# Optimization experiments

Hardware: AMD Instinct MI355X
Metric: run time of the kernel (lower is better)

The kernel has to match this reference:

```python
import jax, jax.numpy as jnp
import numpy as np

N_PE = 100000   # num 'pe' nodes
N_R = 100000    # num 'router' nodes
E = 600000      # edges per relation
D_IN = 64       # input feature dim per node type
H = 128         # hidden_channels
G = 64          # graphs in batch


def setup_inputs() -> dict:
    key = jax.random.key(0)
    ks = jax.random.split(key, 20)
    inp = {}
    inp["x_pe"] = jax.random.normal(ks[0], (N_PE, D_IN), jnp.float32)
    inp["x_r"] = jax.random.normal(ks[1], (N_R, D_IN), jnp.float32)
    # edge_index per relation: row0 = src node ids, row1 = dst node ids
    inp["ei_per"] = jax.random.randint(ks[2], (2, E), 0, N_PE, jnp.int32)   # pe -> router
    inp["ei_rpe"] = jax.random.randint(ks[3], (2, E), 0, N_R, jnp.int32)    # router -> pe
    inp["ei_rr"] = jax.random.randint(ks[4], (2, E), 0, N_R, jnp.int32)     # router -> router
    inp["batch_pe"] = jnp.sort(jax.random.randint(ks[5], (N_PE,), 0, G, jnp.int32))
    inp["batch_r"] = jnp.sort(jax.random.randint(ks[6], (N_R,), 0, G, jnp.int32))
    # GraphConv params, relation axis ordered [pe->router, router->pe, router->router]
    s1 = 1.0 / np.sqrt(D_IN)
    s2 = 1.0 / np.sqrt(H)
    inp["Wrel1"] = jax.random.normal(ks[7], (3, D_IN, H), jnp.float32) * s1
    inp["brel1"] = jnp.zeros((3, H), jnp.float32)
    inp["Wroot1"] = jax.random.normal(ks[8], (3, D_IN, H), jnp.float32) * s1
    inp["Wrel23"] = jax.random.normal(ks[9], (2, 3, H, H), jnp.float32) * s2
    inp["brel23"] = jnp.zeros((2, 3, H), jnp.float32)
    inp["Wroot23"] = jax.random.normal(ks[10], (2, 3, H, H), jnp.float32) * s2
    # per-node-type MLP heads, type axis ordered [pe, router]
    inp["mlp_W1"] = jax.random.normal(ks[11], (2, H, 5), jnp.float32) * s2
    inp["mlp_b1"] = jnp.zeros((2, 5), jnp.float32)
    inp["mlp_W2"] = jax.random.normal(ks[12], (2, 5, 1), jnp.float32) * (1.0 / np.sqrt(5.0))
    inp["mlp_b2"] = jnp.zeros((2, 1), jnp.float32)
    inp["out_W"] = jax.random.normal(ks[13], (2, 1), jnp.float32) * (1.0 / np.sqrt(2.0))
    inp["out_b"] = jnp.zeros((1,), jnp.float32)
    return inp


def _hetero_graphconv(x_pe, x_r, ei_per, ei_rpe, ei_rr, Wrel, brel, Wroot):
    # GraphConv: lin_rel(scatter_add(x_src)) + lin_root(x_dst); to_hetero sums per dst type.
    agg_r_from_pe = jax.ops.segment_sum(x_pe[ei_per[0]], ei_per[1], num_segments=N_R)
    agg_pe_from_r = jax.ops.segment_sum(x_r[ei_rpe[0]], ei_rpe[1], num_segments=N_PE)
    agg_r_from_r = jax.ops.segment_sum(x_r[ei_rr[0]], ei_rr[1], num_segments=N_R)
    o_pe = agg_pe_from_r @ Wrel[1] + brel[1] + x_pe @ Wroot[1]
    o_r = (agg_r_from_pe @ Wrel[0] + brel[0] + x_r @ Wroot[0]) \
        + (agg_r_from_r @ Wrel[2] + brel[2] + x_r @ Wroot[2])
    return o_pe, o_r


def reference(x_pe, x_r, ei_per, ei_rpe, ei_rr, batch_pe, batch_r,
              Wrel1, brel1, Wroot1, Wrel23, brel23, Wroot23,
              mlp_W1, mlp_b1, mlp_W2, mlp_b2, out_W, out_b):
    h_pe, h_r = _hetero_graphconv(x_pe, x_r, ei_per, ei_rpe, ei_rr, Wrel1, brel1, Wroot1)
    h_pe, h_r = jax.nn.relu(h_pe), jax.nn.relu(h_r)
    h_pe, h_r = _hetero_graphconv(h_pe, h_r, ei_per, ei_rpe, ei_rr, Wrel23[0], brel23[0], Wroot23[0])
    h_pe, h_r = jax.nn.relu(h_pe), jax.nn.relu(h_r)
    h_pe, h_r = _hetero_graphconv(h_pe, h_r, ei_per, ei_rpe, ei_rr, Wrel23[1], brel23[1], Wroot23[1])
    gm_pe = jax.ops.segment_max(h_pe, batch_pe, num_segments=G)  # [G, H]
    gm_r = jax.ops.segment_max(h_r, batch_r, num_segments=G)
    def mlp(x, W1, b1, W2, b2):
        return jax.nn.relu(x @ W1 + b1) @ W2 + b2
    o_pe = mlp(gm_pe, mlp_W1[0], mlp_b1[0], mlp_W2[0], mlp_b2[0])  # [G, 1]
    o_r = mlp(gm_r, mlp_W1[1], mlp_b1[1], mlp_W2[1], mlp_b2[1])
    cat = jnp.concatenate([o_pe, o_r], axis=1)  # [G, 2]
    return cat @ out_W + out_b  # [G, 1]
```

## Files before the change

### kernel.cpp

```cpp
#include <hip/hip_runtime.h>
#include <cstddef>
#include <cstdint>

#define DIN 64
#define HID 128
#define NBKMAX 256
#define EPB 8192

typedef _Float16 half4v __attribute__((ext_vector_type(4)));
typedef _Float16 half8v __attribute__((ext_vector_type(8)));
typedef float f32x16 __attribute__((ext_vector_type(16)));

__device__ __forceinline__ unsigned encf(float f) {
    unsigned b = __float_as_uint(f);
    return (b & 0x80000000u) ? ~b : (b | 0x80000000u);
}
__device__ __forceinline__ float decf(unsigned u) {
    unsigned b = (u & 0x80000000u) ? (u & 0x7FFFFFFFu) : ~u;
    return __uint_as_float(b);
}

__global__ void matadd3_k(const float* a0, const float* b0f, float* o0, int n0,
                          const float* a1, const float* b1f, float* o1, int n1,
                          const float* a2, const float* b2f, float* o2, int n2) {
    int r = blockIdx.y;
    const float* a = r == 0 ? a0 : (r == 1 ? a1 : a2);
    const float* b = r == 0 ? b0f : (r == 1 ? b1f : b2f);
    float* o = r == 0 ? o0 : (r == 1 ? o1 : o2);
    int n = r == 0 ? n0 : (r == 1 ? n1 : n2);
    int i = blockIdx.x * 256 + threadIdx.x;
    if (i < n) o[i] = a[i] + b[i];
}

__global__ void conv_x2_k(const float* s0, _Float16* d0, int n40,
                          const float* s1, _Float16* d1, int n41) {
    int r = blockIdx.y;
    const float* s = r == 0 ? s0 : s1;
    _Float16* d = r == 0 ? d0 : d1;
    int n4 = r == 0 ? n40 : n41;
    int i = blockIdx.x * 256 + threadIdx.x;
    if (i >= n4) return;
    float4 v = *reinterpret_cast<const float4*>(&s[i * 4]);
    half4v h;
    h.x = (_Float16)v.x; h.y = (_Float16)v.y; h.z = (_Float16)v.z; h.w = (_Float16)v.w;
    *reinterpret_cast<half4v*>(&d[i * 4]) = h;
}

struct CW { const float* src; _Float16* dst; int K; int total; };
__global__ void conv_w7_k(CW c0, CW c1, CW c2, CW c3, CW c4, CW c5, CW c6) {
    CW J;
    switch (blockIdx.y) {
        case 0: J = c0; break; case 1: J = c1; break; case 2: J = c2; break;
        case 3: J = c3; break; case 4: J = c4; break; case 5: J = c5; break;
        default: J = c6; break;
    }
    int i = blockIdx.x * 256 + threadIdx.x;
    if (i >= J.total) return;
    int m = i / (J.K * HID);
    int rem = i % (J.K * HID);
    int k = rem / HID;
    int col = rem % HID;
    J.dst[(size_t)m * HID * J.K + (size_t)col * J.K + k] = (_Float16)J.src[i];
}

__global__ __launch_bounds__(256) void bhist_k(const int* e0, const int* e1, const int* e2, int E,
                                               int* c0, int* c1, int* c2) {
    int r = blockIdx.y;
    const int* ei = r == 0 ? e0 : (r == 1 ? e1 : e2);
    int* cnt = r == 0 ? c0 : (r == 1 ? c1 : c2);
    __shared__ int sc[NBKMAX];
    int t = threadIdx.x;
    sc[t] = 0;
    __syncthreads();
    int base = blockIdx.x * EPB;
    int n = min(EPB, E - base);
    for (int i = t; i < n; i += 256)
        atomicAdd(&sc[(unsigned)ei[E + base + i] >> 9], 1);
    __syncthreads();
    if (sc[t]) atomicAdd(&cnt[t], sc[t]);
}

__global__ __launch_bounds__(256) void bscan_k(int* c0, int* bb0, int* cu0, int* rp0, int n0,
                                               int* c1, int* bb1, int* cu1, int* rp1, int n1,
                                               int* c2, int* bb2, int* cu2, int* rp2, int n2,
                                               int E) {
    __shared__ int sh[256];
    int t = threadIdx.x;
    for (int r = 0; r < 3; ++r) {
        int* cnt = r == 0 ? c0 : (r == 1 ? c1 : c2);
        int* bb  = r == 0 ? bb0 : (r == 1 ? bb1 : bb2);
        int* cu  = r == 0 ? cu0 : (r == 1 ? cu1 : cu2);
        int* rp  = r == 0 ? rp0 : (r == 1 ? rp1 : rp2);
        int N    = r == 0 ? n0 : (r == 1 ? n1 : n2);
        int v = cnt[t];
        sh[t] = v;
        __syncthreads();
        for (int off = 1; off < 256; off <<= 1) {
            int val = (t >= off) ? sh[t - off] : 0;
            __syncthreads();
            sh[t] += val;
            __syncthreads();
        }
        int ex = sh[t] - v;
        bb[t] = ex;
        cu[t] = ex;
        if (t == 255) bb[256] = sh[255];
        if (t == 0) rp[N] = E;
        __syncthreads();
    }
}

__global__ __launch_bounds__(256) void bin_k(const int* e0, const int* e1, const int* e2, int E,
                                             int* cu0, int* cu1, int* cu2,
                                             unsigned* t0, unsigned* t1, unsigned* t2) {
    int r = blockIdx.y;
    const int* ei = r == 0 ? e0 : (r == 1 ? e1 : e2);
    int* gcur = r == 0 ? cu0 : (r == 1 ? cu1 : cu2);
    unsigned* temp = r == 0 ? t0 : (r == 1 ? t1 : t2);
    __shared__ unsigned pk[EPB];
    __shared__ unsigned short bkb[EPB];
    __shared__ int cnt[NBKMAX];
    __shared__ int scn[NBKMAX];
    __shared__ int rb[NBKMAX];
    int t = threadIdx.x;
    int base = blockIdx.x * EPB;
    int n = min(EPB, E - base);
    cnt[t] = 0;
    __syncthreads();
    for (int i = t; i < n; i += 256)
        atomicAdd(&cnt[(unsigned)ei[E + base + i] >> 9], 1);
    __syncthreads();
    {
        int v = cnt[t];
        scn[t] = v;
        __syncthreads();
        for (int off = 1; off < 256; off <<= 1) {
            int val = (t >= off) ? scn[t - off] : 0;
            __syncthreads();
            scn[t] += val;
            __syncthreads();
        }
        int ex = scn[t] - v;
        __syncthreads();
        scn[t] = ex;
    }
    {
        int c = cnt[t];
        rb[t] = c ? atomicAdd(&gcur[t], c) : 0;
        cnt[t] = 0;
    }
    __syncthreads();
    for (int i = t; i < n; i += 256) {
        int s = ei[base + i];
        int d = ei[E + base + i];
        int b = (unsigned)d >> 9;
        int slot = scn[b] + atomicAdd(&cnt[b], 1);
        pk[slot] = ((unsigned)s << 9) | (unsigned)(d & 511);
        bkb[slot] = (unsigned short)b;
    }
    __syncthreads();
    for (int i = t; i < n; i += 256) {
        int b = bkb[i];
        temp[rb[b] + (i - scn[b])] = pk[i];
    }
}

__global__ __launch_bounds__(256) void bcsr_k(const unsigned* t0, const unsigned* t1, const unsigned* t2,
                                              const int* bb0, const int* bb1, const int* bb2,
                                              int* rp0, int* rp1, int* rp2,
                                              int* a0, int* a1, int* a2,
                                              int n0, int n1, int n2) {
    int r = blockIdx.y;
    const unsigned* temp = r == 0 ? t0 : (r == 1 ? t1 : t2);
    const int* bb = r == 0 ? bb0 : (r == 1 ? bb1 : bb2);
    int* rp = r == 0 ? rp0 : (r == 1 ? rp1 : rp2);
    int* adj = r == 0 ? a0 : (r == 1 ? a1 : a2);
    int N = r == 0 ? n0 : (r == 1 ? n1 : n2);
    int b = blockIdx.x;
    int lo = bb[b], hi = bb[b + 1];
    __shared__ int cnt[512];
    __shared__ int sh[256];
    int t = threadIdx.x;
    cnt[t] = 0; cnt[t + 256] = 0;
    __syncthreads();
    for (int i = lo + t; i < hi; i += 256)
        atomicAdd(&cnt[temp[i] & 511], 1);
    __syncthreads();
    int c0 = cnt[2 * t], c1 = cnt[2 * t + 1];
    sh[t] = c0 + c1;
    __syncthreads();
    for (int off = 1; off < 256; off <<= 1) {
        int v = (t >= off) ? sh[t - off] : 0;
        __syncthreads();
        sh[t] += v;
        __syncthreads();
    }
    int pairExcl = sh[t] - (c0 + c1);
    __syncthreads();
    int e0x = lo + pairExcl;
    int e1x = e0x + c0;
    cnt[2 * t] = e0x;
    cnt[2 * t + 1] = e1x;
    int nodeBase = b * 512;
    if (nodeBase + 2 * t < N) rp[nodeBase + 2 * t] = e0x;
    if (nodeBase + 2 * t + 1 < N) rp[nodeBase + 2 * t + 1] = e1x;
    __syncthreads();
    for (int i = lo + t; i < hi; i += 256) {
        unsigned p = temp[i];
        int pos = atomicAdd(&cnt[p & 511], 1);
        adj[pos] = p >> 9;
    }
}

struct AJob { const _Float16* X; const int* rp; const int* adj; _Float16* AGG; int N; int gb; };
template <int D>
__global__ __launch_bounds__(256) void gather3_k(AJob a0, AJob a1, AJob a2) {
    int b = blockIdx.x;
    AJob J;
    if (b < a0.gb) { J = a0; }
    else if (b < a0.gb + a1.gb) { J = a1; b -= a0.gb; }
    else { J = a2; b -= a0.gb + a1.gb; }
    constexpr int TPN = D / 8;
    constexpr int NPB = 256 / TPN;
    int node = b * NPB + threadIdx.x / TPN;
    int lane = threadIdx.x % TPN;
    if (node >= J.N) return;
    int a = J.rp[node], e1 = J.rp[node + 1];
    float acc[8] = {0.f, 0.f, 0.f, 0.f, 0.f, 0.f, 0.f, 0.f};
    int e = a;
    for (; e + 2 <= e1; e += 2) {
        int s0 = J.adj[e], s1 = J.adj[e + 1];
        half8v v0 = *reinterpret_cast<const half8v*>(&J.X[(size_t)s0 * D + lane * 8]);
        half8v v1 = *reinterpret_cast<const half8v*>(&J.X[(size_t)s1 * D + lane * 8]);
#pragma unroll
        for (int i = 0; i < 8; ++i) acc[i] += (float)v0[i];
#pragma unroll
        for (int i = 0; i < 8; ++i) acc[i] += (float)v1[i];
    }
    if (e < e1) {
        int s0 = J.adj[e];
        half8v v0 = *reinterpret_cast<const half8v*>(&J.X[(size_t)s0 * D + lane * 8]);
#pragma unroll
        for (int i = 0; i < 8; ++i) acc[i] += (float)v0[i];
    }
    half8v o;
#pragma unroll
    for (int i = 0; i < 8; ++i) o[i] = (_Float16)acc[i];
    *reinterpret_cast<half8v*>(&J.AGG[(size_t)node * D + lane * 8]) = o;
}

struct GJob {
    const _Float16* A0; const _Float16* A1; const _Float16* A2;
    const _Float16* W0; const _Float16* W1; const _Float16* W2;
    const float* b0; const float* b1;
    _Float16* O;
    int N; int total; int gb;
};

template <bool RELU>
__global__ __launch_bounds__(256) void gemm2_k(GJob j0, GJob j1, int K, int lg) {
    const bool second = ((int)blockIdx.x >= j0.gb);
    const GJob J = second ? j1 : j0;
    const int bx = blockIdx.x - (second ? j0.gb : 0);
    __shared__ _Float16 Alds[2][128 * 32];
    const int tid = threadIdx.x;
    const int lane = tid & 63;
    const int w = tid >> 6;
    const int wr = w & 1, wc = w >> 1;
    const int rowBase = bx * 128;

    f32x16 acc[2][2];
#pragma unroll
    for (int r = 0; r < 2; ++r)
#pragma unroll
        for (int c = 0; c < 2; ++c)
#pragma unroll
            for (int q = 0; q < 16; ++q) acc[r][c][q] = 0.0f;

    const _Float16* Ap[3] = {J.A0, J.A1, J.A2};

    const int srow = tid & 127;
    const int skh = (tid >> 7) * 16;
    const int gr = rowBase + srow;
    const bool rowOK = (gr < J.N);
    const int sR = (srow >> 5) * 2 + (skh >> 4);
    const int sl5 = srow & 31;
    const int off0 = (sR * 64 + sl5) * 8;
    const int off1 = (sR * 64 + sl5 + 32) * 8;

    const int total = J.total;
    const int cmask = (1 << lg) - 1;

    auto ld = [&](int c, half8v& h0, half8v& h1) {
        int s = c >> lg;
        int k0 = (c & cmask) * 32;
        half8v z = {};
        h0 = z; h1 = z;
        if (rowOK) {
            const _Float16* p = Ap[s] + (size_t)gr * K + k0 + skh;
            h0 = *reinterpret_cast<const half8v*>(p);
            h1 = *reinterpret_cast<const half8v*>(p + 8);
        }
    };

    half8v pa, pb, na, nb, fa, fb;
    ld(0, pa, pb);
    *reinterpret_cast<half8v*>(&Alds[0][off0]) = pa;
    *reinterpret_cast<half8v*>(&Alds[0][off1]) = pb;
    if (total > 1) ld(1, na, nb);
    __syncthreads();

    for (int c = 0; c < total; ++c) {
        if (c + 2 < total) ld(c + 2, fa, fb);
        int s = c >> lg;
        int k0 = (c & cmask) * 32;
        const _Float16* __restrict__ Wt = (s == 0) ? J.W0 : (s == 1 ? J.W1 : J.W2);
        const _Float16* buf = Alds[c & 1];
#pragma unroll
        for (int t = 0; t < 2; ++t) {
            half8v av[2], wv[2];
#pragma unroll
            for (int r = 0; r < 2; ++r) {
                int R = (wr * 2 + r) * 2 + t;
                av[r] = *reinterpret_cast<const half8v*>(&buf[(R * 64 + lane) * 8]);
            }
#pragma unroll
            for (int cc = 0; cc < 2; ++cc) {
                int col = wc * 64 + cc * 32 + (lane & 31);
                wv[cc] = *reinterpret_cast<const half8v*>(
                    &Wt[(size_t)col * K + k0 + t * 16 + (lane >> 5) * 8]);
            }
#pragma unroll
            for (int r = 0; r < 2; ++r)
#pragma unroll
                for (int cc = 0; cc < 2; ++cc)
                    acc[r][cc] = __builtin_amdgcn_mfma_f32_32x32x16_f16(wv[cc], av[r], acc[r][cc], 0, 0, 0);
        }
        if (c + 1 < total) {
            _Float16* nbuf = Alds[(c + 1) & 1];
            *reinterpret_cast<half8v*>(&nbuf[off0]) = na;
            *reinterpret_cast<half8v*>(&nbuf[off1]) = nb;
        }
        __syncthreads();
        na = fa; nb = fb;
    }

#pragma unroll
    for (int r = 0; r < 2; ++r) {
        int node = rowBase + (wr * 2 + r) * 32 + (lane & 31);
        if (node >= J.N) continue;
        _Float16* orow = J.O + (size_t)node * HID;
#pragma unroll
        for (int cc = 0; cc < 2; ++cc) {
            int fb_ = wc * 64 + cc * 32 + 4 * (lane >> 5);
#pragma unroll
            for (int g = 0; g < 4; ++g) {
                int f = fb_ + g * 8;
                float4 bv = *reinterpret_cast<const float4*>(&J.b0[f]);
                if (J.b1) {
                    float4 b2v = *reinterpret_cast<const float4*>(&J.b1[f]);
                    bv.x += b2v.x; bv.y += b2v.y; bv.z += b2v.z; bv.w += b2v.w;
                }
                half4v hv;
#pragma unroll
                for (int i = 0; i < 4; ++i) {
                    float v = acc[r][cc][g * 4 + i] + ((const float*)&bv)[i];
                    if (RELU) v = fmaxf(v, 0.f);
                    hv[i] = (_Float16)v;
                }
                *reinterpret_cast<half4v*>(&orow[f]) = hv;
            }
        }
    }
}

__global__ void seg_bounds2_k(const int* b0, int n0, int* s0,
                              const int* b1, int n1, int* s1, int G) {
    int r = blockIdx.x;
    const int* batch = r == 0 ? b0 : b1;
    int n = r == 0 ? n0 : n1;
    int* starts = r == 0 ? s0 : s1;
    int g = threadIdx.x;
    if (g > G) return;
    int lo = 0, hi = n;
    while (lo < hi) {
        int mid = (lo + hi) >> 1;
        if (batch[mid] < g) lo = mid + 1; else hi = mid;
    }
    starts[g] = lo;
}

__global__ __launch_bounds__(128) void seg_max2_k(const _Float16* H0, const int* st0, unsigned* g0,
                                                  const _Float16* H1, const int* st1, unsigned* g1) {
    int z = blockIdx.z;
    const _Float16* Hf = z == 0 ? H0 : H1;
    const int* starts = z == 0 ? st0 : st1;
    unsigned* gmU = z == 0 ? g0 : g1;
    int g = blockIdx.x;
    int sub = blockIdx.y;
    int SUB = gridDim.y;
    int f = threadIdx.x;
    int s0 = starts[g], s1 = starts[g + 1];
    int len = s1 - s0;
    if (len <= 0) return;
    int chunk = (len + SUB - 1) / SUB;
    int a = s0 + sub * chunk;
    int b = min(a + chunk, s1);
    if (a >= b) return;
    float m = -__builtin_huge_valf();
    for (int n = a; n < b; ++n) m = fmaxf(m, (float)Hf[(size_t)n * HID + f]);
    atomicMax(&gmU[g * HID + f], encf(m));
}

__global__ void head_k(const unsigned* __restrict__ gmU_pe, const unsigned* __restrict__ gmU_r,
                       const float* __restrict__ W1, const float* __restrict__ b1,
                       const float* __restrict__ W2, const float* __restrict__ b2,
                       const float* __restrict__ oW, const float* __restrict__ ob,
                       float* __restrict__ out, int G) {
    int g = threadIdx.x;
    if (g >= G) return;
    float vals[2];
#pragma unroll
    for (int t = 0; t < 2; ++t) {
        const unsigned* gm = t ? gmU_r : gmU_pe;
        float z[5];
#pragma unroll
        for (int j = 0; j < 5; ++j) z[j] = b1[t * 5 + j];
        for (int f = 0; f < HID; ++f) {
            float x = decf(gm[g * HID + f]);
#pragma unroll
            for (int j = 0; j < 5; ++j) z[j] = fmaf(x, W1[t * HID * 5 + f * 5 + j], z[j]);
        }
        float o = b2[t];
#pragma unroll
        for (int j = 0; j < 5; ++j) o = fmaf(fmaxf(z[j], 0.f), W2[t * 5 + j], o);
        vals[t] = o;
    }
    out[g] = vals[0] * oW[0] + vals[1] * oW[1] + ob[0];
}

extern "C" void kernel_launch(void* const* d_in, const int* in_sizes, int n_in,
                              void* d_out, int out_size, void* d_ws, size_t ws_size,
                              hipStream_t stream) {
    const float* x_pe    = (const float*)d_in[0];
    const float* x_r     = (const float*)d_in[1];
    const int* ei_per    = (const int*)d_in[2];
    const int* ei_rpe    = (const int*)d_in[3];
    const int* ei_rr     = (const int*)d_in[4];
    const int* batch_pe  = (const int*)d_in[5];
    const int* batch_r   = (const int*)d_in[6];
    const float* Wrel1   = (const float*)d_in[7];
    const float* brel1   = (const float*)d_in[8];
    const float* Wroot1  = (const float*)d_in[9];
    const float* Wrel23  = (const float*)d_in[10];
    const float* brel23  = (const float*)d_in[11];
    const float* Wroot23 = (const float*)d_in[12];
    const float* mlp_W1  = (const float*)d_in[13];
    const float* mlp_b1  = (const float*)d_in[14];
    const float* mlp_W2  = (const float*)d_in[15];
    const float* mlp_b2  = (const float*)d_in[16];
    const float* out_W   = (const float*)d_in[17];
    const float* out_b   = (const float*)d_in[18];
    float* out = (float*)d_out;

    const int N_PE = in_sizes[0] / DIN;
    const int N_R  = in_sizes[1] / DIN;
    const int E    = in_sizes[2] / 2;
    const int G    = out_size;
    const int NMAX = (N_PE > N_R) ? N_PE : N_R;
    const size_t SZM = (size_t)NMAX * HID;

    _Float16* H1 = (_Float16*)d_ws;
    _Float16* H2 = H1 + SZM;
    _Float16* H3 = H2 + SZM;
    _Float16* H4 = H3 + SZM;
    _Float16* H5 = H4 + SZM;
    _Float16* xh_pe = H5 + SZM;
    _Float16* xh_r  = xh_pe + (size_t)N_PE * DIN;
    float* wsum1 = (float*)(xh_r + (size_t)N_R * DIN);
    float* wsum2 = wsum1 + DIN * HID;
    float* wsum3 = wsum2 + HID * HID;
    _Float16* wt_rel1    = (_Float16*)(wsum3 + HID * HID);
    _Float16* wt_root1pe = wt_rel1 + 3 * DIN * HID;
    _Float16* wt_wsum1   = wt_root1pe + DIN * HID;
    _Float16* wt_rel23   = wt_wsum1 + DIN * HID;
    _Float16* wt_root23  = wt_rel23 + 6 * HID * HID;
    _Float16* wt_wsum2   = wt_root23 + 6 * HID * HID;
    _Float16* wt_wsum3   = wt_wsum2 + HID * HID;
    unsigned* gmU_pe = (unsigned*)(wt_wsum3 + HID * HID);
    unsigned* gmU_r  = gmU_pe + G * HID;
    int* starts_pe = (int*)(gmU_r + G * HID);
    int* starts_r  = starts_pe + (G + 1);
    int* bktCnt = starts_r + (G + 1);
    int* bb     = bktCnt + 3 * NBKMAX;
    int* gcur   = bb + 3 * (NBKMAX + 1);
    int* csr    = gcur + 3 * NBKMAX;
    const size_t relstride = (size_t)(NMAX + 1) + 2 * (size_t)E + 16;

    int* rp[3]; int* adjp[3]; unsigned* tmp[3];
    const int Nds[3] = {N_R, N_PE, N_R};
    for (int r = 0; r < 3; ++r) {
        int* rowptr = csr + (size_t)r * relstride;
        rp[r] = rowptr;
        adjp[r] = rowptr + (Nds[r] + 1);
        tmp[r] = (unsigned*)(adjp[r] + E);
    }

    const int gpe = (N_PE + 127) / 128, grr = (N_R + 127) / 128;

    {
        dim3 g((16384 + 255) / 256, 3);
        matadd3_k<<<g, 256, 0, stream>>>(
            Wroot1, Wroot1 + 2 * DIN * HID, wsum1, DIN * HID,
            Wroot23, Wroot23 + 2 * HID * HID, wsum2, HID * HID,
            Wroot23 + 3 * HID * HID, Wroot23 + 5 * HID * HID, wsum3, HID * HID);
    }
    {
        int n40 = N_PE * DIN / 4, n41 = N_R * DIN / 4;
        int nmax = n40 > n41 ? n40 : n41;
        dim3 g((nmax + 255) / 256, 2);
        conv_x2_k<<<g, 256, 0, stream>>>(x_pe, xh_pe, n40, x_r, xh_r, n41);
    }
    {
        CW c0{Wrel1, wt_rel1, DIN, 3 * DIN * HID};
        CW c1{Wroot1 + 1 * DIN * HID, wt_root1pe, DIN, DIN * HID};
        CW c2{wsum1, wt_wsum1, DIN, DIN * HID};
        CW c3{Wrel23, wt_rel23, HID, 6 * HID * HID};
        CW c4{Wroot23, wt_root23, HID, 6 * HID * HID};
        CW c5{wsum2, wt_wsum2, HID, HID * HID};
        CW c6{wsum3, wt_wsum3, HID, HID * HID};
        dim3 g((6 * HID * HID + 255) / 256, 7);
        conv_w7_k<<<g, 256, 0, stream>>>(c0, c1, c2, c3, c4, c5, c6);
    }
    {
        hipMemsetAsync(bktCnt, 0, 3 * NBKMAX * sizeof(int), stream);
        int eb = (E + EPB - 1) / EPB;
        dim3 gh(eb, 3);
        bhist_k<<<gh, 256, 0, stream>>>(ei_per, ei_rpe, ei_rr, E,
                                        bktCnt, bktCnt + NBKMAX, bktCnt + 2 * NBKMAX);
        bscan_k<<<1, 256, 0, stream>>>(
            bktCnt, bb, gcur, rp[0], Nds[0],
            bktCnt + NBKMAX, bb + (NBKMAX + 1), gcur + NBKMAX, rp[1], Nds[1],
            bktCnt + 2 * NBKMAX, bb + 2 * (NBKMAX + 1), gcur + 2 * NBKMAX, rp[2], Nds[2], E);
        bin_k<<<gh, 256, 0, stream>>>(ei_per, ei_rpe, ei_rr, E,
                                      gcur, gcur + NBKMAX, gcur + 2 * NBKMAX,
                                      tmp[0], tmp[1], tmp[2]);
        dim3 gc(NBKMAX, 3);
        bcsr_k<<<gc, 256, 0, stream>>>(tmp[0], tmp[1], tmp[2],
                                       bb, bb + (NBKMAX + 1), bb + 2 * (NBKMAX + 1),
                                       rp[0], rp[1], rp[2],
                                       adjp[0], adjp[1], adjp[2],
                                       Nds[0], Nds[1], Nds[2]);
    }

    {
        AJob a0{xh_r, rp[1], adjp[1], H1, N_PE, (N_PE + 31) / 32};
        AJob a1{xh_pe, rp[0], adjp[0], H2, N_R, (N_R + 31) / 32};
        AJob a2{xh_r, rp[2], adjp[2], H3, N_R, (N_R + 31) / 32};
        gather3_k<DIN><<<a0.gb + a1.gb + a2.gb, 256, 0, stream>>>(a0, a1, a2);
        GJob jp{H1, xh_pe, nullptr,
                wt_rel1 + 1 * DIN * HID, wt_root1pe, nullptr,
                brel1 + HID, nullptr, H4, N_PE, 2 * 2, gpe};
        GJob jr{H2, H3, xh_r,
                wt_rel1, wt_rel1 + 2 * DIN * HID, wt_wsum1,
                brel1, brel1 + 2 * HID, H5, N_R, 3 * 2, grr};
        gemm2_k<true><<<gpe + grr, 256, 0, stream>>>(jp, jr, DIN, 1);
    }
    {
        AJob a0{H5, rp[1], adjp[1], H1, N_PE, (N_PE + 15) / 16};
        AJob a1{H4, rp[0], adjp[0], H2, N_R, (N_R + 15) / 16};
        AJob a2{H5, rp[2], adjp[2], H3, N_R, (N_R + 15) / 16};
        gather3_k<HID><<<a0.gb + a1.gb + a2.gb, 256, 0, stream>>>(a0, a1, a2);
        GJob jp{H1, H4, nullptr,
                wt_rel23 + 1 * HID * HID, wt_root23 + 1 * HID * HID, nullptr,
                brel23 + HID, nullptr, H1, N_PE, 2 * 4, gpe};
        GJob jr{H2, H3, H5,
                wt_rel23, wt_rel23 + 2 * HID * HID, wt_wsum2,
                brel23, brel23 + 2 * HID, H2, N_R, 3 * 4, grr};
        gemm2_k<true><<<gpe + grr, 256, 0, stream>>>(jp, jr, HID, 2);
    }
    {
        AJob a0{H2, rp[1], adjp[1], H3, N_PE, (N_PE + 15) / 16};
        AJob a1{H1, rp[0], adjp[0], H4, N_R, (N_R + 15) / 16};
        AJob a2{H2, rp[2], adjp[2], H5, N_R, (N_R + 15) / 16};
        gather3_k<HID><<<a0.gb + a1.gb + a2.gb, 256, 0, stream>>>(a0, a1, a2);
        GJob jp{H3, H1, nullptr,
                wt_rel23 + 4 * HID * HID, wt_root23 + 4 * HID * HID, nullptr,
                brel23 + 4 * HID, nullptr, H3, N_PE, 2 * 4, gpe};
        GJob jr{H4, H5, H2,
                wt_rel23 + 3 * HID * HID, wt_rel23 + 5 * HID * HID, wt_wsum3,
                brel23 + 3 * HID, brel23 + 5 * HID, H4, N_R, 3 * 4, grr};
        gemm2_k<false><<<gpe + grr, 256, 0, stream>>>(jp, jr, HID, 2);
    }

    seg_bounds2_k<<<2, 128, 0, stream>>>(batch_pe, N_PE, starts_pe, batch_r, N_R, starts_r, G);
    hipMemsetAsync(gmU_pe, 0, 2 * (size_t)G * HID * sizeof(unsigned), stream);
    dim3 gs(G, 16, 2);
    seg_max2_k<<<gs, 128, 0, stream>>>(H3, starts_pe, gmU_pe, H4, starts_r, gmU_r);
    head_k<<<1, 64, 0, stream>>>(gmU_pe, gmU_r, mlp_W1, mlp_b1, mlp_W2, mlp_b2, out_W, out_b, out, G);
}
```

Before: 643.2 us.

## Widen GEMM K-chunk to 64, unroll gather by four, shrink EPB

The GEMM kernel now stages 64-wide K chunks in LDS instead of 32, which halves the number of chunk iterations and barriers. Its prefetch depth drops from two chunks ahead to one, and the launch parameters are updated to the new chunk counts. The gather loop is unrolled to four edges per iteration to keep more independent loads in flight. EPB, which sets edges per block in CSR construction, drops from 8192 to 2048 for more parallelism. In exchange, LDS use doubles, which may reduce occupancy, and the shallower prefetch may expose more global-load latency.

```diff
diff --git a/kernel.cpp b/kernel.cpp
--- a/kernel.cpp
+++ b/kernel.cpp
@@ -5,7 +5,7 @@
 #define DIN 64
 #define HID 128
 #define NBKMAX 256
-#define EPB 8192
+#define EPB 2048
 
 typedef _Float16 half4v __attribute__((ext_vector_type(4)));
 typedef _Float16 half8v __attribute__((ext_vector_type(8)));
@@ -228,16 +228,16 @@
     int a = J.rp[node], e1 = J.rp[node + 1];
     float acc[8] = {0.f, 0.f, 0.f, 0.f, 0.f, 0.f, 0.f, 0.f};
     int e = a;
-    for (; e + 2 <= e1; e += 2) {
-        int s0 = J.adj[e], s1 = J.adj[e + 1];
+    for (; e + 4 <= e1; e += 4) {
+        int s0 = J.adj[e], s1 = J.adj[e + 1], s2 = J.adj[e + 2], s3 = J.adj[e + 3];
         half8v v0 = *reinterpret_cast<const half8v*>(&J.X[(size_t)s0 * D + lane * 8]);
         half8v v1 = *reinterpret_cast<const half8v*>(&J.X[(size_t)s1 * D + lane * 8]);
-#pragma unroll
-        for (int i = 0; i < 8; ++i) acc[i] += (float)v0[i];
-#pragma unroll
-        for (int i = 0; i < 8; ++i) acc[i] += (float)v1[i];
-    }
-    if (e < e1) {
+        half8v v2 = *reinterpret_cast<const half8v*>(&J.X[(size_t)s2 * D + lane * 8]);
+        half8v v3 = *reinterpret_cast<const half8v*>(&J.X[(size_t)s3 * D + lane * 8]);
+#pragma unroll
+        for (int i = 0; i < 8; ++i) acc[i] += (float)v0[i] + (float)v1[i] + (float)v2[i] + (float)v3[i];
+    }
+    for (; e < e1; ++e) {
         int s0 = J.adj[e];
         half8v v0 = *reinterpret_cast<const half8v*>(&J.X[(size_t)s0 * D + lane * 8]);
 #pragma unroll
@@ -262,7 +262,7 @@
     const bool second = ((int)blockIdx.x >= j0.gb);
     const GJob J = second ? j1 : j0;
     const int bx = blockIdx.x - (second ? j0.gb : 0);
-    __shared__ _Float16 Alds[2][128 * 32];
+    __shared__ _Float16 Alds[2][128 * 64];
     const int tid = threadIdx.x;
     const int lane = tid & 63;
     const int w = tid >> 6;
@@ -279,56 +279,58 @@
 
     const _Float16* Ap[3] = {J.A0, J.A1, J.A2};
 
-    const int srow = tid & 127;
-    const int skh = (tid >> 7) * 16;
-    const int gr = rowBase + srow;
+    const int row = tid & 127;
+    const int kh = (tid >> 7) * 32;
+    const int gr = rowBase + row;
     const bool rowOK = (gr < J.N);
-    const int sR = (srow >> 5) * 2 + (skh >> 4);
-    const int sl5 = srow & 31;
-    const int off0 = (sR * 64 + sl5) * 8;
-    const int off1 = (sR * 64 + sl5 + 32) * 8;
+    int offW[4];
+#pragma unroll
+    for (int j = 0; j < 4; ++j) {
+        int t = (kh >> 4) + (j >> 1);
+        int k8 = j & 1;
+        offW[j] = (((row >> 5) * 4 + t) * 64 + (row & 31) + 32 * k8) * 8;
+    }
 
     const int total = J.total;
     const int cmask = (1 << lg) - 1;
 
-    auto ld = [&](int c, half8v& h0, half8v& h1) {
+    auto ld = [&](int c, half8v h[4]) {
         int s = c >> lg;
-        int k0 = (c & cmask) * 32;
+        int k0 = (c & cmask) * 64;
         half8v z = {};
-        h0 = z; h1 = z;
+        h[0] = z; h[1] = z; h[2] = z; h[3] = z;
         if (rowOK) {
-            const _Float16* p = Ap[s] + (size_t)gr * K + k0 + skh;
-            h0 = *reinterpret_cast<const half8v*>(p);
-            h1 = *reinterpret_cast<const half8v*>(p + 8);
+            const _Float16* p = Ap[s] + (size_t)gr * K + k0 + kh;
+#pragma unroll
+            for (int j = 0; j < 4; ++j) h[j] = *reinterpret_cast<const half8v*>(p + j * 8);
         }
     };
 
-    half8v pa, pb, na, nb, fa, fb;
-    ld(0, pa, pb);
-    *reinterpret_cast<half8v*>(&Alds[0][off0]) = pa;
-    *reinterpret_cast<half8v*>(&Alds[0][off1]) = pb;
-    if (total > 1) ld(1, na, nb);
+    half8v cur[4], nxt[4];
+    ld(0, cur);
+#pragma unroll
+    for (int j = 0; j < 4; ++j) *reinterpret_cast<half8v*>(&Alds[0][offW[j]]) = cur[j];
     __syncthreads();
 
     for (int c = 0; c < total; ++c) {
-        if (c + 2 < total) ld(c + 2, fa, fb);
+        if (c + 1 < total) ld(c + 1, nxt);
         int s = c >> lg;
-        int k0 = (c & cmask) * 32;
+        int wk0 = (c & cmask) * 64;
         const _Float16* __restrict__ Wt = (s == 0) ? J.W0 : (s == 1 ? J.W1 : J.W2);
         const _Float16* buf = Alds[c & 1];
 #pragma unroll
-        for (int t = 0; t < 2; ++t) {
+        for (int t = 0; t < 4; ++t) {
             half8v av[2], wv[2];
 #pragma unroll
             for (int r = 0; r < 2; ++r) {
-                int R = (wr * 2 + r) * 2 + t;
+                int R = (wr * 2 + r) * 4 + t;
                 av[r] = *reinterpret_cast<const half8v*>(&buf[(R * 64 + lane) * 8]);
             }
 #pragma unroll
             for (int cc = 0; cc < 2; ++cc) {
                 int col = wc * 64 + cc * 32 + (lane & 31);
                 wv[cc] = *reinterpret_cast<const half8v*>(
-                    &Wt[(size_t)col * K + k0 + t * 16 + (lane >> 5) * 8]);
+                    &Wt[(size_t)col * K + wk0 + t * 16 + (lane >> 5) * 8]);
             }
 #pragma unroll
             for (int r = 0; r < 2; ++r)
@@ -337,12 +339,11 @@
                     acc[r][cc] = __builtin_amdgcn_mfma_f32_32x32x16_f16(wv[cc], av[r], acc[r][cc], 0, 0, 0);
         }
         if (c + 1 < total) {
-            _Float16* nbuf = Alds[(c + 1) & 1];
-            *reinterpret_cast<half8v*>(&nbuf[off0]) = na;
-            *reinterpret_cast<half8v*>(&nbuf[off1]) = nb;
+            _Float16* nb = Alds[(c + 1) & 1];
+#pragma unroll
+            for (int j = 0; j < 4; ++j) *reinterpret_cast<half8v*>(&nb[offW[j]]) = nxt[j];
         }
         __syncthreads();
-        na = fa; nb = fb;
     }
 
 #pragma unroll
@@ -560,11 +561,11 @@
         gather3_k<DIN><<<a0.gb + a1.gb + a2.gb, 256, 0, stream>>>(a0, a1, a2);
         GJob jp{H1, xh_pe, nullptr,
                 wt_rel1 + 1 * DIN * HID, wt_root1pe, nullptr,
-                brel1 + HID, nullptr, H4, N_PE, 2 * 2, gpe};
+                brel1 + HID, nullptr, H4, N_PE, 2, gpe};
         GJob jr{H2, H3, xh_r,
                 wt_rel1, wt_rel1 + 2 * DIN * HID, wt_wsum1,
-                brel1, brel1 + 2 * HID, H5, N_R, 3 * 2, grr};
-        gemm2_k<true><<<gpe + grr, 256, 0, stream>>>(jp, jr, DIN, 1);
+                brel1, brel1 + 2 * HID, H5, N_R, 3, grr};
+        gemm2_k<true><<<gpe + grr, 256, 0, stream>>>(jp, jr, DIN, 0);
     }
     {
         AJob a0{H5, rp[1], adjp[1], H1, N_PE, (N_PE + 15) / 16};
@@ -573,11 +574,11 @@
         gather3_k<HID><<<a0.gb + a1.gb + a2.gb, 256, 0, stream>>>(a0, a1, a2);
         GJob jp{H1, H4, nullptr,
                 wt_rel23 + 1 * HID * HID, wt_root23 + 1 * HID * HID, nullptr,
-                brel23 + HID, nullptr, H1, N_PE, 2 * 4, gpe};
+                brel23 + HID, nullptr, H1, N_PE, 2 * 2, gpe};
         GJob jr{H2, H3, H5,
                 wt_rel23, wt_rel23 + 2 * HID * HID, wt_wsum2,
-                brel23, brel23 + 2 * HID, H2, N_R, 3 * 4, grr};
-        gemm2_k<true><<<gpe + grr, 256, 0, stream>>>(jp, jr, HID, 2);
+                brel23, brel23 + 2 * HID, H2, N_R, 3 * 2, grr};
+        gemm2_k<true><<<gpe + grr, 256, 0, stream>>>(jp, jr, HID, 1);
     }
     {
         AJob a0{H2, rp[1], adjp[1], H3, N_PE, (N_PE + 15) / 16};
@@ -586,11 +587,11 @@
         gather3_k<HID><<<a0.gb + a1.gb + a2.gb, 256, 0, stream>>>(a0, a1, a2);
         GJob jp{H3, H1, nullptr,
                 wt_rel23 + 4 * HID * HID, wt_root23 + 4 * HID * HID, nullptr,
-                brel23 + 4 * HID, nullptr, H3, N_PE, 2 * 4, gpe};
+                brel23 + 4 * HID, nullptr, H3, N_PE, 2 * 2, gpe};
         GJob jr{H4, H5, H2,
                 wt_rel23 + 3 * HID * HID, wt_rel23 + 5 * HID * HID, wt_wsum3,
-                brel23 + 3 * HID, brel23 + 5 * HID, H4, N_R, 3 * 4, grr};
-        gemm2_k<false><<<gpe + grr, 256, 0, stream>>>(jp, jr, HID, 2);
+                brel23 + 3 * HID, brel23 + 5 * HID, H4, N_R, 3 * 2, grr};
+        gemm2_k<false><<<gpe + grr, 256, 0, stream>>>(jp, jr, HID, 1);
     }
 
     seg_bounds2_k<<<2, 128, 0, stream>>>(batch_pe, N_PE, starts_pe, batch_r, N_R, starts_r, G);
```

Result: faster. 629.4 us (-2.1%).
